# Optimization experiments

Measured on AMD Instinct MI355X. Metric: run time of the kernel, lower is better.

Reference implementation:

```python
import jax, jax.numpy as jnp
import numpy as np

D = 1280          # hidden_size
NH = 16           # num_heads
HD = 80           # head_dim
DEPTH = 4         # number of vision blocks
INTER = 3420      # mlp intermediate size
MERGE = 2         # spatial_merge_size
OUT = 3584        # merger out_hidden_size
GRID = (1, 40, 40)  # (t, h, w) patch grid -> 1600 tokens
N = GRID[0] * GRID[1] * GRID[2]
PATCH_IN = 3 * 2 * 14 * 14  # in_channels * temporal_patch * patch^2 = 1176


def _pos_emb():
    """Deterministic vision RoPE cos/sin per Qwen2_5_VLVisionModel.rot_pos_emb."""
    t, h, w = GRID
    mh, mw = h // MERGE, w // MERGE
    intra = np.arange(MERGE)
    row = np.arange(mh)[:, None, None, None] * MERGE + intra[None, None, :, None]
    col = np.arange(mw)[None, :, None, None] * MERGE + intra[None, None, None, :]
    row = np.broadcast_to(row, (mh, mw, MERGE, MERGE)).reshape(-1)
    col = np.broadcast_to(col, (mh, mw, MERGE, MERGE)).reshape(-1)
    pos = np.stack([row, col], axis=-1)        # (h*w, 2)
    if t > 1:
        pos = np.tile(pos, (t, 1))
    rot_dim = HD // 2                          # 40
    inv = 1.0 / (10000.0 ** (np.arange(0, rot_dim, 2, dtype=np.float64) / rot_dim))
    table = np.outer(np.arange(max(h, w)), inv)        # (max_hw, rot_dim//2)
    rpe = table[pos].reshape(pos.shape[0], -1)         # (N, rot_dim)
    emb = np.concatenate([rpe, rpe], axis=-1)          # (N, HD)
    return np.cos(emb).astype(np.float32), np.sin(emb).astype(np.float32)


def setup_inputs() -> dict:
    key = jax.random.key(0)
    ks = iter(jax.random.split(key, 40))
    def w(shape, s=0.02):
        return jax.random.normal(next(ks), shape, jnp.float32) * s
    cos, sin = _pos_emb()
    return dict(
        pixel_values=w((N, PATCH_IN), 1.0),
        cos=jnp.asarray(cos), sin=jnp.asarray(sin),
        patch_w=w((D, PATCH_IN)),                       # Conv3d stride==kernel -> linear
        norm1_w=jnp.ones((DEPTH, D), jnp.float32),
        qkv_w=w((DEPTH, 3 * D, D)), qkv_b=jnp.zeros((DEPTH, 3 * D), jnp.float32),
        proj_w=w((DEPTH, D, D)), proj_b=jnp.zeros((DEPTH, D), jnp.float32),
        norm2_w=jnp.ones((DEPTH, D), jnp.float32),
        gate_w=w((DEPTH, INTER, D)), gate_b=jnp.zeros((DEPTH, INTER), jnp.float32),
        up_w=w((DEPTH, INTER, D)), up_b=jnp.zeros((DEPTH, INTER), jnp.float32),
        down_w=w((DEPTH, D, INTER)), down_b=jnp.zeros((DEPTH, D), jnp.float32),
        lnq_w=jnp.ones((D,), jnp.float32),
        m1_w=w((D * MERGE ** 2, D * MERGE ** 2)), m1_b=jnp.zeros((D * MERGE ** 2,), jnp.float32),
        m2_w=w((OUT, D * MERGE ** 2)), m2_b=jnp.zeros((OUT,), jnp.float32),
    )


def _rms(x, w, eps=1e-6):
    return x * jax.lax.rsqrt(jnp.mean(x * x, axis=-1, keepdims=True) + eps) * w


def _rotate_half(x):
    x1, x2 = jnp.split(x, 2, axis=-1)
    return jnp.concatenate([-x2, x1], axis=-1)


def _forward(pixel_values, cos, sin, patch_w, norm1_w, qkv_w, qkv_b, proj_w, proj_b,
             norm2_w, gate_w, gate_b, up_w, up_b, down_w, down_b,
             lnq_w, m1_w, m1_b, m2_w, m2_b):
    # patch embed: Conv3d with kernel==stride collapses to a linear projection
    x = pixel_values @ patch_w.T                       # (N, D)
    c = cos[:, None, :]                                # (N, 1, HD)
    s = sin[:, None, :]
    scale = HD ** -0.5
    for i in range(DEPTH):
        # --- attention ---
        h = _rms(x, norm1_w[i])
        qkv = (h @ qkv_w[i].T + qkv_b[i]).reshape(N, 3, NH, HD)
        q, k, v = qkv[:, 0], qkv[:, 1], qkv[:, 2]      # (N, NH, HD)
        q = q * c + _rotate_half(q) * s
        k = k * c + _rotate_half(k) * s
        # NOTE: this impl applies NO cu_seqlens window mask -> full dense attention
        aw = jnp.einsum('nhd,mhd->hnm', q, k) * scale  # (NH, N, N)
        aw = jax.nn.softmax(aw.astype(jnp.float32), axis=-1).astype(x.dtype)
        o = jnp.einsum('hnm,mhd->nhd', aw, v).reshape(N, D)
        x = x + o @ proj_w[i].T + proj_b[i]
        # --- mlp (SwiGLU) ---
        h = _rms(x, norm2_w[i])
        g = h @ gate_w[i].T + gate_b[i]
        u = h @ up_w[i].T + up_b[i]
        x = x + (jax.nn.silu(g) * u) @ down_w[i].T + down_b[i]
    # --- patch merger ---
    h = _rms(x, lnq_w).reshape(-1, D * MERGE ** 2)      # (N/4, 5120)
    h = jax.nn.gelu(h @ m1_w.T + m1_b, approximate=False)
    return h @ m2_w.T + m2_b                            # (N/4, OUT)


def reference(pixel_values, cos, sin, patch_w, norm1_w, qkv_w, qkv_b, proj_w, proj_b,
              norm2_w, gate_w, gate_b, up_w, up_b, down_w, down_b,
              lnq_w, m1_w, m1_b, m2_w, m2_b):
    return _forward(pixel_values, cos, sin, patch_w, norm1_w, qkv_w, qkv_b, proj_w,
                    proj_b, norm2_w, gate_w, gate_b, up_w, up_b, down_w, down_b,
                    lnq_w, m1_w, m1_b, m2_w, m2_b)
```

## Files before the change

kernel.cpp:

```cpp
#include <hip/hip_runtime.h>


typedef __bf16 bf16x8 __attribute__((ext_vector_type(8)));
typedef float  f32x4  __attribute__((ext_vector_type(4)));
typedef unsigned short u16;

#define DEV __device__ __forceinline__

DEV u16 f2bf(float f) {
    union { float f; unsigned u; } v; v.f = f;
    unsigned r = v.u + 0x7FFFu + ((v.u >> 16) & 1u);
    return (u16)(r >> 16);
}
DEV float bf2f(u16 b) {
    union { float f; unsigned u; } v; v.u = ((unsigned)b) << 16; return v.f;
}

DEV void gload16(const u16* g, u16* l) {
    __builtin_amdgcn_global_load_lds(
        (const __attribute__((address_space(1))) unsigned int*)g,
        (__attribute__((address_space(3))) unsigned int*)l, 16, 0, 0);
}

enum { EPI_NONE = 0, EPI_BIAS = 1, EPI_BIAS_RESID = 2, EPI_BIAS_GELU = 3, EPI_PART = 4 };

DEV unsigned xcd_map(unsigned lin, unsigned nwg) {
    unsigned q = nwg >> 3, r = nwg & 7, xc = lin & 7, off = lin >> 3;
    return (xc < r ? xc * (q + 1) : r * (q + 1) + (xc - r) * q) + off;
}

__global__ void cvt_kernel(const float* __restrict__ src, u16* __restrict__ dst,
                           int Rs, int Cs, int Rp, int Cp,
                           long long sls, long long dls)
{
    const float* s = src + (size_t)blockIdx.y * sls;
    u16* d = dst + (size_t)blockIdx.y * dls;
    int idx = blockIdx.x * 256 + threadIdx.x;
    int cpc = Cp >> 3;
    if (idx >= Rp * cpc) return;
    int row = idx / cpc;
    int c0  = (idx - row * cpc) * 8;
    u16 v[8];
    if (row < Rs && c0 + 8 <= Cs) {
        float4 a = *reinterpret_cast<const float4*>(&s[(size_t)row * Cs + c0]);
        float4 b = *reinterpret_cast<const float4*>(&s[(size_t)row * Cs + c0 + 4]);
        v[0] = f2bf(a.x); v[1] = f2bf(a.y); v[2] = f2bf(a.z); v[3] = f2bf(a.w);
        v[4] = f2bf(b.x); v[5] = f2bf(b.y); v[6] = f2bf(b.z); v[7] = f2bf(b.w);
    } else {
#pragma unroll
        for (int j = 0; j < 8; ++j) {
            int c = c0 + j;
            v[j] = (row < Rs && c < Cs) ? f2bf(s[(size_t)row * Cs + c]) : (u16)0;
        }
    }
    *reinterpret_cast<uint4*>(&d[(size_t)row * Cp + c0]) =
        *reinterpret_cast<const uint4*>(v);
}

__global__ void gub_kernel(const float* __restrict__ gb, const float* __restrict__ ub,
                           float* __restrict__ dst)
{
    int i = blockIdx.x * 256 + threadIdx.x;
    if (i >= 4 * 6912) return;
    int l = i / 6912, c = i - l * 6912;
    float v = 0.f;
    if (c < 3456) { if (c < 3420) v = gb[l * 3420 + c]; }
    else { int c2 = c - 3456; if (c2 < 3420) v = ub[l * 3420 + c2]; }
    dst[i] = v;
}

template <int EPI, bool OF32>
__global__ __launch_bounds__(256, 3)
void gemm16_kernel(const u16* __restrict__ A, const u16* __restrict__ B,
                   const float* __restrict__ bias, const float* __restrict__ resid,
                   void* __restrict__ outp, int Kp, int ldc, int Rlim,
                   int ktn, size_t zstride)
{
    __shared__ u16 sA[3][4096];
    __shared__ u16 sB[3][4096];
    const int tid  = threadIdx.x;
    const int lane = tid & 63;
    const int w    = tid >> 6;

    const unsigned gy  = gridDim.y;
    const unsigned nwg = gridDim.x * gy;
    const unsigned lin = blockIdx.x + blockIdx.y * gridDim.x;
    const unsigned id2 = xcd_map(lin, nwg);
    const int c0 = (int)(id2 / gy) * 128;
    const int r0 = (int)(id2 - (id2 / gy) * gy) * 128;

    const int wr  = (w >> 1) * 64;
    const int wc  = (w & 1) * 64;
    const int l15 = lane & 15;
    const int kk  = (lane >> 4) * 8;
    const int pco = (((lane >> 4) ^ ((l15 >> 1) & 3)) * 8) - kk;

    const int ca  = w * 128 + lane;
    const int cb  = ca + 64;
    const int sza = ((ca & 3) ^ ((ca >> 3) & 3)) * 8;
    const int szb = ((cb & 3) ^ ((cb >> 3) & 3)) * 8;
    const size_t arow0 = (size_t)(r0 + (ca >> 2)) * Kp + sza;
    const size_t brow0 = (size_t)(c0 + (ca >> 2)) * Kp + sza;
    const size_t arow1 = (size_t)(r0 + (cb >> 2)) * Kp + szb;
    const size_t brow1 = (size_t)(c0 + (cb >> 2)) * Kp + szb;

    f32x4 acc[4][4];
#pragma unroll
    for (int i = 0; i < 4; ++i)
#pragma unroll
        for (int j = 0; j < 4; ++j) acc[i][j] = (f32x4){0.f, 0.f, 0.f, 0.f};

    const int kt0 = blockIdx.z * ktn;
    auto stage = [&](int kt, int buf) {
        int k0 = kt * 32;
        gload16(A + arow0 + k0, &sA[buf][ca * 8]);
        gload16(B + brow0 + k0, &sB[buf][ca * 8]);
        gload16(A + arow1 + k0, &sA[buf][cb * 8]);
        gload16(B + brow1 + k0, &sB[buf][cb * 8]);
    };
    auto compute = [&](int buf) {
        bf16x8 af[4], bfr[4];
#pragma unroll
        for (int f = 0; f < 4; ++f) {
            af[f]  = *reinterpret_cast<const bf16x8*>(&sA[buf][(wr + f * 16 + l15) * 32 + kk + pco]);
            bfr[f] = *reinterpret_cast<const bf16x8*>(&sB[buf][(wc + f * 16 + l15) * 32 + kk + pco]);
        }
#pragma unroll
        for (int fr = 0; fr < 4; ++fr)
#pragma unroll
            for (int fc = 0; fc < 4; ++fc)
                acc[fr][fc] = __builtin_amdgcn_mfma_f32_16x16x32_bf16(af[fr], bfr[fc], acc[fr][fc], 0, 0, 0);
    };

    const int NT = ktn;
    stage(kt0, 0);
    if (NT > 1) stage(kt0 + 1, 1);
    int bcur = 0;
    for (int t = 0; t < NT - 1; ++t) {
        asm volatile("s_waitcnt vmcnt(4)" ::: "memory");
        __builtin_amdgcn_s_barrier();
        __builtin_amdgcn_sched_barrier(0);
        if (t + 2 < NT) {
            int bn = bcur + 2; if (bn >= 3) bn -= 3;
            stage(kt0 + t + 2, bn);
        }
        __builtin_amdgcn_sched_barrier(0);
        compute(bcur);
        bcur = (bcur == 2) ? 0 : bcur + 1;
    }
    asm volatile("s_waitcnt vmcnt(0)" ::: "memory");
    __builtin_amdgcn_s_barrier();
    __builtin_amdgcn_sched_barrier(0);
    compute(bcur);

    const int rowb = r0 + wr + (lane >> 4) * 4;
    const int colb = c0 + wc + l15;
    if (EPI == EPI_PART) {
        float* pp = (float*)outp + (size_t)blockIdx.z * zstride;
#pragma unroll
        for (int fc = 0; fc < 4; ++fc) {
            int col = colb + fc * 16;
#pragma unroll
            for (int fr = 0; fr < 4; ++fr)
#pragma unroll
                for (int r2 = 0; r2 < 4; ++r2)
                    pp[(size_t)(rowb + fr * 16 + r2) * ldc + col] = acc[fr][fc][r2];
        }
        return;
    }
#pragma unroll
    for (int fc = 0; fc < 4; ++fc) {
        int col = colb + fc * 16;
        float bv = (EPI != EPI_NONE) ? bias[col] : 0.f;
#pragma unroll
        for (int fr = 0; fr < 4; ++fr) {
#pragma unroll
            for (int r2 = 0; r2 < 4; ++r2) {
                int row = rowb + fr * 16 + r2;
                if (row >= Rlim) continue;
                float v = acc[fr][fc][r2] + bv;
                if (EPI == EPI_BIAS_RESID) v += resid[(size_t)row * ldc + col];
                if (EPI == EPI_BIAS_GELU)  v = 0.5f * v * (1.f + erff(v * 0.70710678118f));
                if (OF32) ((float*)outp)[(size_t)row * ldc + col] = v;
                else      ((u16*)outp)[(size_t)row * ldc + col] = f2bf(v);
            }
        }
    }
}

template <int EPI, bool OF32>
__global__ __launch_bounds__(256, 4)
void gemm32_kernel(const u16* __restrict__ A, const u16* __restrict__ B,
                   const float* __restrict__ bias, const float* __restrict__ resid,
                   void* __restrict__ outp, int Kp, int ldc, int Rlim)
{
    __shared__ u16 sA[3][1024];
    __shared__ u16 sB[3][4096];
    const int tid  = threadIdx.x;
    const int lane = tid & 63;
    const int w    = tid >> 6;

    const unsigned gy  = gridDim.y;
    const unsigned nwg = gridDim.x * gy;
    const unsigned lin = blockIdx.x + blockIdx.y * gridDim.x;
    const unsigned id2 = xcd_map(lin, nwg);
    const int c0 = (int)(id2 / gy) * 128;
    const int r0 = (int)(id2 - (id2 / gy) * gy) * 32;

    const int wc  = w * 32;
    const int l15 = lane & 15;
    const int kk  = (lane >> 4) * 8;
    const int pco = (((lane >> 4) ^ ((l15 >> 1) & 3)) * 8) - kk;

    const int cB0 = tid, cB1 = tid + 256, cA = tid & 127;
    const size_t bsrc0 = (size_t)(c0 + (cB0 >> 2)) * Kp + ((cB0 & 3) ^ ((cB0 >> 3) & 3)) * 8;
    const size_t bsrc1 = (size_t)(c0 + (cB1 >> 2)) * Kp + ((cB1 & 3) ^ ((cB1 >> 3) & 3)) * 8;
    const size_t asrc  = (size_t)(r0 + (cA  >> 2)) * Kp + ((cA  & 3) ^ ((cA  >> 3) & 3)) * 8;

    f32x4 acc[2][2];
#pragma unroll
    for (int i = 0; i < 2; ++i)
#pragma unroll
        for (int j = 0; j < 2; ++j) acc[i][j] = (f32x4){0.f, 0.f, 0.f, 0.f};

    auto stage = [&](int kt, int buf) {
        int k0 = kt * 32;
        gload16(B + bsrc0 + k0, &sB[buf][cB0 * 8]);
        gload16(B + bsrc1 + k0, &sB[buf][cB1 * 8]);
        gload16(A + asrc  + k0, &sA[buf][cA * 8]);
    };
    auto compute = [&](int buf) {
        bf16x8 af[2], bfr[2];
#pragma unroll
        for (int f = 0; f < 2; ++f) {
            af[f]  = *reinterpret_cast<const bf16x8*>(&sA[buf][(f * 16 + l15) * 32 + kk + pco]);
            bfr[f] = *reinterpret_cast<const bf16x8*>(&sB[buf][(wc + f * 16 + l15) * 32 + kk + pco]);
        }
#pragma unroll
        for (int fr = 0; fr < 2; ++fr)
#pragma unroll
            for (int fc = 0; fc < 2; ++fc)
                acc[fr][fc] = __builtin_amdgcn_mfma_f32_16x16x32_bf16(af[fr], bfr[fc], acc[fr][fc], 0, 0, 0);
    };

    const int NT = Kp >> 5;
    stage(0, 0);
    stage(1, 1);
    int bcur = 0;
    for (int t = 0; t < NT - 1; ++t) {
        asm volatile("s_waitcnt vmcnt(3)" ::: "memory");
        __builtin_amdgcn_s_barrier();
        __builtin_amdgcn_sched_barrier(0);
        if (t + 2 < NT) {
            int bn = bcur + 2; if (bn >= 3) bn -= 3;
            stage(t + 2, bn);
        }
        __builtin_amdgcn_sched_barrier(0);
        compute(bcur);
        bcur = (bcur == 2) ? 0 : bcur + 1;
    }
    asm volatile("s_waitcnt vmcnt(0)" ::: "memory");
    __builtin_amdgcn_s_barrier();
    __builtin_amdgcn_sched_barrier(0);
    compute(bcur);

    const int rowb = r0 + (lane >> 4) * 4;
    const int colb = c0 + wc + l15;
#pragma unroll
    for (int fc = 0; fc < 2; ++fc) {
        int col = colb + fc * 16;
        float bv = (EPI != EPI_NONE) ? bias[col] : 0.f;
#pragma unroll
        for (int fr = 0; fr < 2; ++fr) {
#pragma unroll
            for (int r2 = 0; r2 < 4; ++r2) {
                int row = rowb + fr * 16 + r2;
                if (row >= Rlim) continue;
                float v = acc[fr][fc][r2] + bv;
                if (EPI == EPI_BIAS_RESID) v += resid[(size_t)row * ldc + col];
                if (EPI == EPI_BIAS_GELU)  v = 0.5f * v * (1.f + erff(v * 0.70710678118f));
                if (OF32) ((float*)outp)[(size_t)row * ldc + col] = v;
                else      ((u16*)outp)[(size_t)row * ldc + col] = f2bf(v);
            }
        }
    }
}

template <int GELU, bool OF32>
__global__ void reduce_kernel(const float* __restrict__ part, const float* __restrict__ bias,
                              void* __restrict__ outp, int C, int S, size_t zstride, int total4)
{
    int i = blockIdx.x * 256 + threadIdx.x;
    if (i >= total4) return;
    int cq = C >> 2;
    int rr = i / cq;
    int cc = (i - rr * cq) * 4;
    size_t bidx = (size_t)rr * C + cc;
    float4 s = *reinterpret_cast<const float4*>(&part[bidx]);
    for (int z = 1; z < S; ++z) {
        float4 p = *reinterpret_cast<const float4*>(&part[z * zstride + bidx]);
        s.x += p.x; s.y += p.y; s.z += p.z; s.w += p.w;
    }
    float4 b = *reinterpret_cast<const float4*>(&bias[cc]);
    s.x += b.x; s.y += b.y; s.z += b.z; s.w += b.w;
    if (GELU) {
        s.x = 0.5f * s.x * (1.f + erff(s.x * 0.70710678118f));
        s.y = 0.5f * s.y * (1.f + erff(s.y * 0.70710678118f));
        s.z = 0.5f * s.z * (1.f + erff(s.z * 0.70710678118f));
        s.w = 0.5f * s.w * (1.f + erff(s.w * 0.70710678118f));
    }
    if (OF32) {
        *reinterpret_cast<float4*>(&((float*)outp)[bidx]) = s;
    } else {
        u16 v[4] = { f2bf(s.x), f2bf(s.y), f2bf(s.z), f2bf(s.w) };
        *reinterpret_cast<uint2*>(&((u16*)outp)[bidx]) = *reinterpret_cast<const uint2*>(v);
    }
}

__global__ void rms_kernel(const float* __restrict__ x, const float* __restrict__ w,
                           u16* __restrict__ out, int cols)
{
    const int row = blockIdx.x;
    const int tid = threadIdx.x;
    const float* xr = x + (size_t)row * cols;
    float ss = 0.f;
    for (int c = tid; c < cols; c += 256) { float v = xr[c]; ss += v * v; }
#pragma unroll
    for (int m = 1; m < 64; m <<= 1) ss += __shfl_xor(ss, m);
    __shared__ float wsum[4];
    if ((tid & 63) == 0) wsum[tid >> 6] = ss;
    __syncthreads();
    float tot = wsum[0] + wsum[1] + wsum[2] + wsum[3];
    float rs = rsqrtf(tot / (float)cols + 1e-6f);
    u16* orow = out + (size_t)row * cols;
    for (int c = tid; c < cols; c += 256) orow[c] = f2bf(xr[c] * rs * w[c]);
}

__global__ void rope_kernel(u16* __restrict__ qkv, const float* __restrict__ cosb,
                            const float* __restrict__ sinb)
{
    int idx = blockIdx.x * 256 + threadIdx.x;
    int n   = idx / 640;
    int rem = idx - n * 640;
    int hh  = rem / 40;
    int d   = rem - hh * 40;
    float c0 = cosb[n * 80 + d];
    float s0 = sinb[n * 80 + d];
    float c1 = cosb[n * 80 + d + 40];
    float s1 = sinb[n * 80 + d + 40];
    size_t base = (size_t)n * 3840 + hh * 80;
    float a = bf2f(qkv[base + d]), b = bf2f(qkv[base + d + 40]);
    qkv[base + d]      = f2bf(a * c0 - b * s0);
    qkv[base + d + 40] = f2bf(b * c1 + a * s1);
    base += 1280;
    a = bf2f(qkv[base + d]); b = bf2f(qkv[base + d + 40]);
    qkv[base + d]      = f2bf(a * c0 - b * s0);
    qkv[base + d + 40] = f2bf(b * c1 + a * s1);
}

__global__ void silu_mul_kernel(const u16* __restrict__ gu, u16* __restrict__ outb)
{
    int idx = blockIdx.x * 256 + threadIdx.x;
    if (idx >= 1664 * 432) return;
    int row = idx / 432, c8 = (idx - row * 432) * 8;
    u16 gv[8], uv[8];
    *reinterpret_cast<uint4*>(gv) = *reinterpret_cast<const uint4*>(&gu[(size_t)row * 6912 + c8]);
    *reinterpret_cast<uint4*>(uv) = *reinterpret_cast<const uint4*>(&gu[(size_t)row * 6912 + 3456 + c8]);
#pragma unroll
    for (int j = 0; j < 8; ++j) {
        float x = bf2f(gv[j]);
        gv[j] = f2bf(x / (1.f + __expf(-x)) * bf2f(uv[j]));
    }
    *reinterpret_cast<uint4*>(&outb[(size_t)row * 3456 + c8]) = *reinterpret_cast<const uint4*>(gv);
}

__global__ __launch_bounds__(256, 2)
void attn_kernel(const u16* __restrict__ qkv, u16* __restrict__ o)
{
    __shared__ __align__(16) u16      Klds[2][64][104];
    __shared__ __align__(16) unsigned Vt32[2][80][36];
    __shared__ __align__(16) u16      Plds[4][16][72];
    const int tid  = threadIdx.x;
    const int lane = tid & 63;
    const int w    = tid >> 6;
    const int l15  = lane & 15;
    const int kk   = (lane >> 4) * 8;
    unsigned lin = blockIdx.y * 25 + blockIdx.x;
    unsigned id2 = (lin & 7) * 50 + (lin >> 3);
    const int hh = (int)(id2 / 25);
    const int qt = (int)(id2 - hh * 25);
    const float scale = 0.11180339887498949f;

    const int koff = 1280 + hh * 80;
    const int voff = 2560 + hh * 80;

    {
        int r  = tid >> 2;
        int cq = 80 + (tid & 3) * 4;
        *reinterpret_cast<uint2*>(&Klds[0][r][cq]) = make_uint2(0u, 0u);
        *reinterpret_cast<uint2*>(&Klds[1][r][cq]) = make_uint2(0u, 0u);
    }

    const int qrow = qt * 64 + w * 16 + l15;
    bf16x8 aq[3];
#pragma unroll
    for (int s = 0; s < 3; ++s) {
        int d = 32 * s + kk;
        union { bf16x8 v; uint4 q; } uu;
        if (d < 80) uu.q = *reinterpret_cast<const uint4*>(&qkv[(size_t)qrow * 3840 + hh * 80 + d]);
        else        uu.q = make_uint4(0u, 0u, 0u, 0u);
        aq[s] = uu.v;
    }

    const int kc0 = tid, kc1 = tid + 256, kc2 = tid + 512;
    const int kr0 = kc0 / 10, k80 = (kc0 - kr0 * 10) * 8;
    const int kr1 = kc1 / 10, k81 = (kc1 - kr1 * 10) * 8;
    const int kr2 = kc2 / 10, k82 = (kc2 - kr2 * 10) * 8;
    const size_t ksrc0 = (size_t)kr0 * 3840 + koff + k80;
    const size_t ksrc1 = (size_t)kr1 * 3840 + koff + k81;
    const size_t ksrc2 = (size_t)kr2 * 3840 + koff + k82;
    const int rpA = tid & 31, gA = tid >> 5;
    const int gB = 8 + (tid >> 5);
    const size_t vsrcA = (size_t)(2 * rpA) * 3840 + voff + gA * 8;
    const size_t vsrcB = (size_t)(2 * rpA) * 3840 + voff + gB * 8;

    uint4 kg0, kg1, kg2, va0, va1, vb0, vb1;
    auto LOADR = [&](int kb) {
        size_t tb = (size_t)kb * 245760;
        kg0 = *reinterpret_cast<const uint4*>(&qkv[tb + ksrc0]);
        kg1 = *reinterpret_cast<const uint4*>(&qkv[tb + ksrc1]);
        if (tid < 128) kg2 = *reinterpret_cast<const uint4*>(&qkv[tb + ksrc2]);
        va0 = *reinterpret_cast<const uint4*>(&qkv[tb + vsrcA]);
        va1 = *reinterpret_cast<const uint4*>(&qkv[tb + vsrcA + 3840]);
        if (tid < 64) {
            vb0 = *reinterpret_cast<const uint4*>(&qkv[tb + vsrcB]);
            vb1 = *reinterpret_cast<const uint4*>(&qkv[tb + vsrcB + 3840]);
        }
    };
    auto STORE = [&](int b) {
        *reinterpret_cast<uint4*>(&Klds[b][kr0][k80]) = kg0;
        *reinterpret_cast<uint4*>(&Klds[b][kr1][k81]) = kg1;
        if (tid < 128) *reinterpret_cast<uint4*>(&Klds[b][kr2][k82]) = kg2;
        union { uint4 q; u16 h[8]; } xa0, xa1;
        xa0.q = va0; xa1.q = va1;
#pragma unroll
        for (int j = 0; j < 8; ++j)
            Vt32[b][gA * 8 + j][rpA] = (unsigned)xa0.h[j] | ((unsigned)xa1.h[j] << 16);
        if (tid < 64) {
            union { uint4 q; u16 h[8]; } xb0, xb1;
            xb0.q = vb0; xb1.q = vb1;
#pragma unroll
            for (int j = 0; j < 8; ++j)
                Vt32[b][gB * 8 + j][rpA] = (unsigned)xb0.h[j] | ((unsigned)xb1.h[j] << 16);
        }
    };

    f32x4 acc_o[5];
#pragma unroll
    for (int fd = 0; fd < 5; ++fd) acc_o[fd] = (f32x4){0.f, 0.f, 0.f, 0.f};
    float m[4], lsum[4];
#pragma unroll
    for (int r2 = 0; r2 < 4; ++r2) { m[r2] = -__builtin_inff(); lsum[r2] = 0.f; }

    LOADR(0);
    STORE(0);
    __syncthreads();
    int cur = 0;

    for (int kb = 0; kb < 25; ++kb) {
        if (kb < 24) LOADR(kb + 1);

        f32x4 sf[4];
#pragma unroll
        for (int fc = 0; fc < 4; ++fc) {
            f32x4 c = (f32x4){0.f, 0.f, 0.f, 0.f};
#pragma unroll
            for (int s = 0; s < 3; ++s)
                c = __builtin_amdgcn_mfma_f32_16x16x32_bf16(
                        aq[s],
                        *reinterpret_cast<const bf16x8*>(&Klds[cur][fc * 16 + l15][32 * s + kk]),
                        c, 0, 0, 0);
            sf[fc] = c * scale;
        }

        float mx[4];
#pragma unroll
        for (int r2 = 0; r2 < 4; ++r2)
            mx[r2] = fmaxf(fmaxf(sf[0][r2], sf[1][r2]), fmaxf(sf[2][r2], sf[3][r2]));
#pragma unroll
        for (int msk = 1; msk <= 8; msk <<= 1)
#pragma unroll
            for (int r2 = 0; r2 < 4; ++r2)
                mx[r2] = fmaxf(mx[r2], __shfl_xor(mx[r2], msk));
        float alpha[4];
#pragma unroll
        for (int r2 = 0; r2 < 4; ++r2) {
            float mn = fmaxf(m[r2], mx[r2]);
            alpha[r2] = __expf(m[r2] - mn);
            m[r2] = mn;
        }
        float psum[4] = {0.f, 0.f, 0.f, 0.f};
#pragma unroll
        for (int fc = 0; fc < 4; ++fc)
#pragma unroll
            for (int r2 = 0; r2 < 4; ++r2) {
                float p = __expf(sf[fc][r2] - m[r2]);
                sf[fc][r2] = p;
                psum[r2] += p;
            }
#pragma unroll
        for (int msk = 1; msk <= 8; msk <<= 1)
#pragma unroll
            for (int r2 = 0; r2 < 4; ++r2) psum[r2] += __shfl_xor(psum[r2], msk);
#pragma unroll
        for (int r2 = 0; r2 < 4; ++r2) lsum[r2] = lsum[r2] * alpha[r2] + psum[r2];
#pragma unroll
        for (int fd = 0; fd < 5; ++fd)
#pragma unroll
            for (int r2 = 0; r2 < 4; ++r2) acc_o[fd][r2] *= alpha[r2];

        const int prow = (lane >> 4) * 4;
#pragma unroll
        for (int fc = 0; fc < 4; ++fc)
#pragma unroll
            for (int r2 = 0; r2 < 4; ++r2)
                Plds[w][prow + r2][fc * 16 + l15] = f2bf(sf[fc][r2]);

        bf16x8 ap[2];
#pragma unroll
        for (int ks = 0; ks < 2; ++ks)
            ap[ks] = *reinterpret_cast<const bf16x8*>(&Plds[w][l15][32 * ks + kk]);
#pragma unroll
        for (int fd = 0; fd < 5; ++fd) {
            const u16* vrow = reinterpret_cast<const u16*>(&Vt32[cur][fd * 16 + l15][0]);
#pragma unroll
            for (int ks = 0; ks < 2; ++ks)
                acc_o[fd] = __builtin_amdgcn_mfma_f32_16x16x32_bf16(
                        ap[ks],
                        *reinterpret_cast<const bf16x8*>(&vrow[32 * ks + kk]),
                        acc_o[fd], 0, 0, 0);
        }

        if (kb < 24) STORE(cur ^ 1);
        __syncthreads();
        cur ^= 1;
    }

    float inv[4];
#pragma unroll
    for (int r2 = 0; r2 < 4; ++r2) inv[r2] = 1.f / lsum[r2];
    const int orow = qt * 64 + w * 16 + (lane >> 4) * 4;
    const int ocol = hh * 80 + l15;
#pragma unroll
    for (int fd = 0; fd < 5; ++fd)
#pragma unroll
        for (int r2 = 0; r2 < 4; ++r2)
            o[(size_t)(orow + r2) * 1280 + ocol + fd * 16] = f2bf(acc_o[fd][r2] * inv[r2]);
}

extern "C" void kernel_launch(void* const* d_in, const int* in_sizes, int n_in,
                              void* d_out, int out_size, void* d_ws, size_t ws_size,
                              hipStream_t stream)
{
    const float* pixel  = (const float*)d_in[0];
    const float* cosb   = (const float*)d_in[1];
    const float* sinb   = (const float*)d_in[2];
    const float* patchw = (const float*)d_in[3];
    const float* n1w    = (const float*)d_in[4];
    const float* qkvw   = (const float*)d_in[5];
    const float* qkvb   = (const float*)d_in[6];
    const float* projw  = (const float*)d_in[7];
    const float* projb  = (const float*)d_in[8];
    const float* n2w    = (const float*)d_in[9];
    const float* gatew  = (const float*)d_in[10];
    const float* gateb  = (const float*)d_in[11];
    const float* upw    = (const float*)d_in[12];
    const float* upb    = (const float*)d_in[13];
    const float* downw  = (const float*)d_in[14];
    const float* downb  = (const float*)d_in[15];
    const float* lnqw   = (const float*)d_in[16];
    const float* m1w    = (const float*)d_in[17];
    const float* m1b    = (const float*)d_in[18];
    const float* m2w    = (const float*)d_in[19];
    const float* m2b    = (const float*)d_in[20];
    float* out = (float*)d_out;

    char* base = (char*)d_ws;
    float* x      = (float*)(base);
    u16*   h      = (u16*)(base + 8519680);
    u16*   qbuf   = (u16*)(base + 12779520);
    u16*   pix16  = qbuf;
    u16*   gsep   = (u16*)(base + 25559040);
    u16*   o      = gsep;
    u16*   pw16   = gsep;
    u16*   gu     = (u16*)(base + 37060608);
    u16*   t1     = gu;
    float* guB    = (float*)(base + 60063744);
    u16*   qkvw16 = (u16*)(base + 60174336);
    u16*   projw16= (u16*)(base + 99495936);
    u16*   guw16  = (u16*)(base + 112603136);
    u16*   downw16= (u16*)(base + 183382016);
    u16*   m1w16  = guw16;
    u16*   m2w16  = (u16*)(base + 112603136 + 52428800);
    float* part   = (float*)qkvw16;

    dim3 blk(256);
    auto cvb = [](int Rp, int Cp) { return (Rp * (Cp >> 3) + 255) / 256; };

    cvt_kernel<<<dim3(cvb(1664,1216),1), blk, 0, stream>>>(pixel, pix16, 1600, 1176, 1664, 1216, 0, 0);
    cvt_kernel<<<dim3(cvb(1280,1216),1), blk, 0, stream>>>(patchw, pw16, 1280, 1176, 1280, 1216, 0, 0);
    cvt_kernel<<<dim3(cvb(15360,1280),1), blk, 0, stream>>>(qkvw, qkvw16, 15360, 1280, 15360, 1280, 0, 0);
    cvt_kernel<<<dim3(cvb(5120,1280),1), blk, 0, stream>>>(projw, projw16, 5120, 1280, 5120, 1280, 0, 0);
    cvt_kernel<<<dim3(cvb(3456,1280),4), blk, 0, stream>>>(gatew, guw16, 3420, 1280, 3456, 1280, 4377600LL, 8847360LL);
    cvt_kernel<<<dim3(cvb(3456,1280),4), blk, 0, stream>>>(upw, guw16 + 4423680, 3420, 1280, 3456, 1280, 4377600LL, 8847360LL);
    cvt_kernel<<<dim3(cvb(1280,3456),4), blk, 0, stream>>>(downw, downw16, 1280, 3420, 1280, 3456, 4377600LL, 4423680LL);
    gub_kernel<<<108, blk, 0, stream>>>(gateb, upb, guB);

    gemm32_kernel<EPI_NONE, true><<<dim3(10,52), blk, 0, stream>>>(pix16, pw16, nullptr, nullptr, x, 1216, 1280, 1664);
    for (int i = 0; i < 4; ++i) {
        rms_kernel<<<1600, blk, 0, stream>>>(x, n1w + i*1280, h, 1280);
        gemm16_kernel<EPI_BIAS, false><<<dim3(30,13), blk, 0, stream>>>(h, qkvw16 + (size_t)i*4915200, qkvb + i*3840, nullptr, qbuf, 1280, 3840, 1664, 40, 0);
        rope_kernel<<<4000, blk, 0, stream>>>(qbuf, cosb, sinb);
        attn_kernel<<<dim3(25,16), blk, 0, stream>>>(qbuf, o);
        gemm32_kernel<EPI_BIAS_RESID, true><<<dim3(10,52), blk, 0, stream>>>(o, projw16 + (size_t)i*1638400, projb + i*1280, x, x, 1280, 1280, 1664);
        rms_kernel<<<1600, blk, 0, stream>>>(x, n2w + i*1280, h, 1280);
        gemm16_kernel<EPI_BIAS, false><<<dim3(54,13), blk, 0, stream>>>(h, guw16 + (size_t)i*8847360, guB + i*6912, nullptr, gu, 1280, 6912, 1664, 40, 0);
        silu_mul_kernel<<<2808, blk, 0, stream>>>(gu, gsep);
        gemm32_kernel<EPI_BIAS_RESID, true><<<dim3(10,52), blk, 0, stream>>>(gsep, downw16 + (size_t)i*4423680, downb + i*1280, x, x, 3456, 1280, 1664);
    }
    cvt_kernel<<<dim3(cvb(5120,5120),1), blk, 0, stream>>>(m1w, m1w16, 5120, 5120, 5120, 5120, 0, 0);
    cvt_kernel<<<dim3(cvb(3584,5120),1), blk, 0, stream>>>(m2w, m2w16, 3584, 5120, 3584, 5120, 0, 0);
    rms_kernel<<<1600, blk, 0, stream>>>(x, lnqw, h, 1280);
    gemm16_kernel<EPI_PART, false><<<dim3(40,4,5), blk, 0, stream>>>(h, m1w16, nullptr, nullptr, part, 5120, 5120, 512, 32, 2621440);
    reduce_kernel<1, false><<<2560, blk, 0, stream>>>(part, m1b, t1, 5120, 5, 2621440, 655360);
    gemm16_kernel<EPI_PART, false><<<dim3(28,4,5), blk, 0, stream>>>(t1, m2w16, nullptr, nullptr, part, 5120, 3584, 512, 32, 1835008);
    reduce_kernel<0, true><<<1400, blk, 0, stream>>>(part, m2b, out, 3584, 5, 1835008, 358400);
}
```

Measured before the change: 1.293 ms.

## Fuse fp32-to-bf16 weight conversion into GEMM B-tile loads

Removes the separate weight conversion kernels. The GEMMs now read fp32 weights directly, convert them to bf16 in registers and write them to shared memory. The A operand still uses async global-to-LDS loads, but the pipeline drops from triple to double buffering with plain __syncthreads. This saves a full pass that reads fp32 weights and writes bf16 copies. In exchange, each GEMM must read weights at twice the bytes, and every block that shares a weight tile repeats the conversion. Padded rows and columns are handled by predicated loads and zero fill.

```diff
diff --git a/kernel.cpp b/kernel.cpp
--- a/kernel.cpp
+++ b/kernel.cpp
@@ -30,11 +30,8 @@
 }
 
 __global__ void cvt_kernel(const float* __restrict__ src, u16* __restrict__ dst,
-                           int Rs, int Cs, int Rp, int Cp,
-                           long long sls, long long dls)
-{
-    const float* s = src + (size_t)blockIdx.y * sls;
-    u16* d = dst + (size_t)blockIdx.y * dls;
+                           int Rs, int Cs, int Rp, int Cp)
+{
     int idx = blockIdx.x * 256 + threadIdx.x;
     int cpc = Cp >> 3;
     if (idx >= Rp * cpc) return;
@@ -42,18 +39,18 @@
     int c0  = (idx - row * cpc) * 8;
     u16 v[8];
     if (row < Rs && c0 + 8 <= Cs) {
-        float4 a = *reinterpret_cast<const float4*>(&s[(size_t)row * Cs + c0]);
-        float4 b = *reinterpret_cast<const float4*>(&s[(size_t)row * Cs + c0 + 4]);
+        float4 a = *reinterpret_cast<const float4*>(&src[(size_t)row * Cs + c0]);
+        float4 b = *reinterpret_cast<const float4*>(&src[(size_t)row * Cs + c0 + 4]);
         v[0] = f2bf(a.x); v[1] = f2bf(a.y); v[2] = f2bf(a.z); v[3] = f2bf(a.w);
         v[4] = f2bf(b.x); v[5] = f2bf(b.y); v[6] = f2bf(b.z); v[7] = f2bf(b.w);
     } else {
 #pragma unroll
         for (int j = 0; j < 8; ++j) {
             int c = c0 + j;
-            v[j] = (row < Rs && c < Cs) ? f2bf(s[(size_t)row * Cs + c]) : (u16)0;
-        }
-    }
-    *reinterpret_cast<uint4*>(&d[(size_t)row * Cp + c0]) =
+            v[j] = (row < Rs && c < Cs) ? f2bf(src[(size_t)row * Cs + c]) : (u16)0;
+        }
+    }
+    *reinterpret_cast<uint4*>(&dst[(size_t)row * Cp + c0]) =
         *reinterpret_cast<const uint4*>(v);
 }
 
@@ -71,13 +68,15 @@
 
 template <int EPI, bool OF32>
 __global__ __launch_bounds__(256, 3)
-void gemm16_kernel(const u16* __restrict__ A, const u16* __restrict__ B,
-                   const float* __restrict__ bias, const float* __restrict__ resid,
-                   void* __restrict__ outp, int Kp, int ldc, int Rlim,
-                   int ktn, size_t zstride)
-{
-    __shared__ u16 sA[3][4096];
-    __shared__ u16 sB[3][4096];
+void gemm16f_kernel(const u16* __restrict__ A, const float* __restrict__ B0,
+                    const float* __restrict__ B1, int Bsplit, int BvalidRows,
+                    int KpA, int Klog,
+                    const float* __restrict__ bias, const float* __restrict__ resid,
+                    void* __restrict__ outp, int ldc, int Rlim,
+                    int ktn, size_t zstride)
+{
+    __shared__ u16 sA[2][4096];
+    __shared__ u16 sB[2][4096];
     const int tid  = threadIdx.x;
     const int lane = tid & 63;
     const int w    = tid >> 6;
@@ -95,14 +94,25 @@
     const int kk  = (lane >> 4) * 8;
     const int pco = (((lane >> 4) ^ ((l15 >> 1) & 3)) * 8) - kk;
 
-    const int ca  = w * 128 + lane;
-    const int cb  = ca + 64;
-    const int sza = ((ca & 3) ^ ((ca >> 3) & 3)) * 8;
-    const int szb = ((cb & 3) ^ ((cb >> 3) & 3)) * 8;
-    const size_t arow0 = (size_t)(r0 + (ca >> 2)) * Kp + sza;
-    const size_t brow0 = (size_t)(c0 + (ca >> 2)) * Kp + sza;
-    const size_t arow1 = (size_t)(r0 + (cb >> 2)) * Kp + szb;
-    const size_t brow1 = (size_t)(c0 + (cb >> 2)) * Kp + szb;
+    const int ca0 = tid, ca1 = tid + 256;
+    const int ar0 = ca0 >> 2, ar1 = ca1 >> 2;
+    const int alq0 = ((ca0 & 3) ^ ((ar0 >> 1) & 3)) * 8;
+    const int alq1 = ((ca1 & 3) ^ ((ar1 >> 1) & 3)) * 8;
+    const size_t asrc0 = (size_t)(r0 + ar0) * KpA + alq0;
+    const size_t asrc1 = (size_t)(r0 + ar1) * KpA + alq1;
+
+    const int cb0 = tid, cb1 = tid + 256;
+    const int br0 = cb0 >> 2, br1 = cb1 >> 2;
+    const int blq0 = ((cb0 & 3) ^ ((br0 >> 1) & 3)) * 8;
+    const int blq1 = ((cb1 & 3) ^ ((br1 >> 1) & 3)) * 8;
+    bool bv0, bv1;
+    const float *bp0, *bp1;
+    {
+        int gr = c0 + br0; int hs = gr >= Bsplit; int lr = gr - (hs ? Bsplit : 0);
+        bv0 = lr < BvalidRows; bp0 = (hs ? B1 : B0) + (size_t)lr * Klog + blq0;
+        gr = c0 + br1; hs = gr >= Bsplit; lr = gr - (hs ? Bsplit : 0);
+        bv1 = lr < BvalidRows; bp1 = (hs ? B1 : B0) + (size_t)lr * Klog + blq1;
+    }
 
     f32x4 acc[4][4];
 #pragma unroll
@@ -111,19 +121,36 @@
         for (int j = 0; j < 4; ++j) acc[i][j] = (f32x4){0.f, 0.f, 0.f, 0.f};
 
     const int kt0 = blockIdx.z * ktn;
-    auto stage = [&](int kt, int buf) {
+    float4 f00, f01, f10, f11;
+    auto LOADB = [&](int kt) {
         int k0 = kt * 32;
-        gload16(A + arow0 + k0, &sA[buf][ca * 8]);
-        gload16(B + brow0 + k0, &sB[buf][ca * 8]);
-        gload16(A + arow1 + k0, &sA[buf][cb * 8]);
-        gload16(B + brow1 + k0, &sB[buf][cb * 8]);
-    };
-    auto compute = [&](int buf) {
+        if (bv0) { f00 = *reinterpret_cast<const float4*>(bp0 + k0);
+                   f01 = *reinterpret_cast<const float4*>(bp0 + k0 + 4); }
+        else     { f00 = make_float4(0.f,0.f,0.f,0.f); f01 = f00; }
+        if (bv1) { f10 = *reinterpret_cast<const float4*>(bp1 + k0);
+                   f11 = *reinterpret_cast<const float4*>(bp1 + k0 + 4); }
+        else     { f10 = make_float4(0.f,0.f,0.f,0.f); f11 = f10; }
+    };
+    auto WRITEB = [&](int s) {
+        u16 h8[8];
+        h8[0]=f2bf(f00.x); h8[1]=f2bf(f00.y); h8[2]=f2bf(f00.z); h8[3]=f2bf(f00.w);
+        h8[4]=f2bf(f01.x); h8[5]=f2bf(f01.y); h8[6]=f2bf(f01.z); h8[7]=f2bf(f01.w);
+        *reinterpret_cast<uint4*>(&sB[s][cb0 * 8]) = *reinterpret_cast<const uint4*>(h8);
+        h8[0]=f2bf(f10.x); h8[1]=f2bf(f10.y); h8[2]=f2bf(f10.z); h8[3]=f2bf(f10.w);
+        h8[4]=f2bf(f11.x); h8[5]=f2bf(f11.y); h8[6]=f2bf(f11.z); h8[7]=f2bf(f11.w);
+        *reinterpret_cast<uint4*>(&sB[s][cb1 * 8]) = *reinterpret_cast<const uint4*>(h8);
+    };
+    auto stageA = [&](int kt, int s) {
+        int k0 = kt * 32;
+        gload16(A + asrc0 + k0, &sA[s][ca0 * 8]);
+        gload16(A + asrc1 + k0, &sA[s][ca1 * 8]);
+    };
+    auto compute = [&](int s) {
         bf16x8 af[4], bfr[4];
 #pragma unroll
         for (int f = 0; f < 4; ++f) {
-            af[f]  = *reinterpret_cast<const bf16x8*>(&sA[buf][(wr + f * 16 + l15) * 32 + kk + pco]);
-            bfr[f] = *reinterpret_cast<const bf16x8*>(&sB[buf][(wc + f * 16 + l15) * 32 + kk + pco]);
+            af[f]  = *reinterpret_cast<const bf16x8*>(&sA[s][(wr + f * 16 + l15) * 32 + kk + pco]);
+            bfr[f] = *reinterpret_cast<const bf16x8*>(&sB[s][(wc + f * 16 + l15) * 32 + kk + pco]);
         }
 #pragma unroll
         for (int fr = 0; fr < 4; ++fr)
@@ -133,25 +160,20 @@
     };
 
     const int NT = ktn;
-    stage(kt0, 0);
-    if (NT > 1) stage(kt0 + 1, 1);
-    int bcur = 0;
-    for (int t = 0; t < NT - 1; ++t) {
-        asm volatile("s_waitcnt vmcnt(4)" ::: "memory");
-        __builtin_amdgcn_s_barrier();
-        __builtin_amdgcn_sched_barrier(0);
-        if (t + 2 < NT) {
-            int bn = bcur + 2; if (bn >= 3) bn -= 3;
-            stage(kt0 + t + 2, bn);
-        }
-        __builtin_amdgcn_sched_barrier(0);
-        compute(bcur);
-        bcur = (bcur == 2) ? 0 : bcur + 1;
-    }
-    asm volatile("s_waitcnt vmcnt(0)" ::: "memory");
-    __builtin_amdgcn_s_barrier();
-    __builtin_amdgcn_sched_barrier(0);
-    compute(bcur);
+    LOADB(kt0);
+    stageA(kt0, 0);
+    WRITEB(0);
+    stageA(kt0 + 1, 1);
+    LOADB(kt0 + 1);
+    __syncthreads();
+    int s = 0;
+    for (int t = 0; t < NT; ++t) {
+        compute(s);
+        if (t + 1 < NT) WRITEB(s ^ 1);
+        __syncthreads();
+        if (t + 2 < NT) { stageA(kt0 + t + 2, s); LOADB(kt0 + t + 2); }
+        s ^= 1;
+    }
 
     const int rowb = r0 + wr + (lane >> 4) * 4;
     const int colb = c0 + wc + l15;
@@ -190,12 +212,13 @@
 
 template <int EPI, bool OF32>
 __global__ __launch_bounds__(256, 4)
-void gemm32_kernel(const u16* __restrict__ A, const u16* __restrict__ B,
-                   const float* __restrict__ bias, const float* __restrict__ resid,
-                   void* __restrict__ outp, int Kp, int ldc, int Rlim)
-{
-    __shared__ u16 sA[3][1024];
-    __shared__ u16 sB[3][4096];
+void gemm32f_kernel(const u16* __restrict__ A, const float* __restrict__ B,
+                    int KpA, int Klog,
+                    const float* __restrict__ bias, const float* __restrict__ resid,
+                    void* __restrict__ outp, int ldc, int Rlim)
+{
+    __shared__ u16 sA[2][1024];
+    __shared__ u16 sB[2][4096];
     const int tid  = threadIdx.x;
     const int lane = tid & 63;
     const int w    = tid >> 6;
@@ -212,10 +235,17 @@
     const int kk  = (lane >> 4) * 8;
     const int pco = (((lane >> 4) ^ ((l15 >> 1) & 3)) * 8) - kk;
 
-    const int cB0 = tid, cB1 = tid + 256, cA = tid & 127;
-    const size_t bsrc0 = (size_t)(c0 + (cB0 >> 2)) * Kp + ((cB0 & 3) ^ ((cB0 >> 3) & 3)) * 8;
-    const size_t bsrc1 = (size_t)(c0 + (cB1 >> 2)) * Kp + ((cB1 & 3) ^ ((cB1 >> 3) & 3)) * 8;
-    const size_t asrc  = (size_t)(r0 + (cA  >> 2)) * Kp + ((cA  & 3) ^ ((cA  >> 3) & 3)) * 8;
+    const int ca = tid & 127;
+    const int aro = ca >> 2;
+    const int alq = ((ca & 3) ^ ((aro >> 1) & 3)) * 8;
+    const size_t asrc = (size_t)(r0 + aro) * KpA + alq;
+
+    const int cb0 = tid, cb1 = tid + 256;
+    const int br0 = cb0 >> 2, br1 = cb1 >> 2;
+    const int blq0 = ((cb0 & 3) ^ ((br0 >> 1) & 3)) * 8;
+    const int blq1 = ((cb1 & 3) ^ ((br1 >> 1) & 3)) * 8;
+    const float* bp0 = B + (size_t)(c0 + br0) * Klog;
+    const float* bp1 = B + (size_t)(c0 + br1) * Klog;
 
     f32x4 acc[2][2];
 #pragma unroll
@@ -223,18 +253,42 @@
 #pragma unroll
         for (int j = 0; j < 2; ++j) acc[i][j] = (f32x4){0.f, 0.f, 0.f, 0.f};
 
-    auto stage = [&](int kt, int buf) {
+    float4 f00, f01, f10, f11;
+    auto ldchunk = [&](const float* bp, int ks, float4& a, float4& b) {
+        if (ks + 8 <= Klog) {
+            a = *reinterpret_cast<const float4*>(bp + ks);
+            b = *reinterpret_cast<const float4*>(bp + ks + 4);
+        } else {
+            float t[8];
+#pragma unroll
+            for (int e = 0; e < 8; ++e) t[e] = (ks + e < Klog) ? bp[ks + e] : 0.f;
+            a = make_float4(t[0], t[1], t[2], t[3]);
+            b = make_float4(t[4], t[5], t[6], t[7]);
+        }
+    };
+    auto LOADB = [&](int kt) {
         int k0 = kt * 32;
-        gload16(B + bsrc0 + k0, &sB[buf][cB0 * 8]);
-        gload16(B + bsrc1 + k0, &sB[buf][cB1 * 8]);
-        gload16(A + asrc  + k0, &sA[buf][cA * 8]);
-    };
-    auto compute = [&](int buf) {
+        ldchunk(bp0, k0 + blq0, f00, f01);
+        ldchunk(bp1, k0 + blq1, f10, f11);
+    };
+    auto WRITEB = [&](int s) {
+        u16 h8[8];
+        h8[0]=f2bf(f00.x); h8[1]=f2bf(f00.y); h8[2]=f2bf(f00.z); h8[3]=f2bf(f00.w);
+        h8[4]=f2bf(f01.x); h8[5]=f2bf(f01.y); h8[6]=f2bf(f01.z); h8[7]=f2bf(f01.w);
+        *reinterpret_cast<uint4*>(&sB[s][cb0 * 8]) = *reinterpret_cast<const uint4*>(h8);
+        h8[0]=f2bf(f10.x); h8[1]=f2bf(f10.y); h8[2]=f2bf(f10.z); h8[3]=f2bf(f10.w);
+        h8[4]=f2bf(f11.x); h8[5]=f2bf(f11.y); h8[6]=f2bf(f11.z); h8[7]=f2bf(f11.w);
+        *reinterpret_cast<uint4*>(&sB[s][cb1 * 8]) = *reinterpret_cast<const uint4*>(h8);
+    };
+    auto stageA = [&](int kt, int s) {
+        if (tid < 128) gload16(A + asrc + kt * 32, &sA[s][ca * 8]);
+    };
+    auto compute = [&](int s) {
         bf16x8 af[2], bfr[2];
 #pragma unroll
         for (int f = 0; f < 2; ++f) {
-            af[f]  = *reinterpret_cast<const bf16x8*>(&sA[buf][(f * 16 + l15) * 32 + kk + pco]);
-            bfr[f] = *reinterpret_cast<const bf16x8*>(&sB[buf][(wc + f * 16 + l15) * 32 + kk + pco]);
+            af[f]  = *reinterpret_cast<const bf16x8*>(&sA[s][(f * 16 + l15) * 32 + kk + pco]);
+            bfr[f] = *reinterpret_cast<const bf16x8*>(&sB[s][(wc + f * 16 + l15) * 32 + kk + pco]);
         }
 #pragma unroll
         for (int fr = 0; fr < 2; ++fr)
@@ -243,26 +297,21 @@
                 acc[fr][fc] = __builtin_amdgcn_mfma_f32_16x16x32_bf16(af[fr], bfr[fc], acc[fr][fc], 0, 0, 0);
     };
 
-    const int NT = Kp >> 5;
-    stage(0, 0);
-    stage(1, 1);
-    int bcur = 0;
-    for (int t = 0; t < NT - 1; ++t) {
-        asm volatile("s_waitcnt vmcnt(3)" ::: "memory");
-        __builtin_amdgcn_s_barrier();
-        __builtin_amdgcn_sched_barrier(0);
-        if (t + 2 < NT) {
-            int bn = bcur + 2; if (bn >= 3) bn -= 3;
-            stage(t + 2, bn);
-        }
-        __builtin_amdgcn_sched_barrier(0);
-        compute(bcur);
-        bcur = (bcur == 2) ? 0 : bcur + 1;
-    }
-    asm volatile("s_waitcnt vmcnt(0)" ::: "memory");
-    __builtin_amdgcn_s_barrier();
-    __builtin_amdgcn_sched_barrier(0);
-    compute(bcur);
+    const int NT = KpA >> 5;
+    LOADB(0);
+    stageA(0, 0);
+    WRITEB(0);
+    stageA(1, 1);
+    LOADB(1);
+    __syncthreads();
+    int s = 0;
+    for (int t = 0; t < NT; ++t) {
+        compute(s);
+        if (t + 1 < NT) WRITEB(s ^ 1);
+        __syncthreads();
+        if (t + 2 < NT) { stageA(t + 2, s); LOADB(t + 2); }
+        s ^= 1;
+    }
 
     const int rowb = r0 + (lane >> 4) * 4;
     const int colb = c0 + wc + l15;
@@ -586,53 +635,51 @@
     float* out = (float*)d_out;
 
     char* base = (char*)d_ws;
-    float* x      = (float*)(base);
-    u16*   h      = (u16*)(base + 8519680);
-    u16*   qbuf   = (u16*)(base + 12779520);
-    u16*   pix16  = qbuf;
-    u16*   gsep   = (u16*)(base + 25559040);
-    u16*   o      = gsep;
-    u16*   pw16   = gsep;
-    u16*   gu     = (u16*)(base + 37060608);
-    u16*   t1     = gu;
-    float* guB    = (float*)(base + 60063744);
-    u16*   qkvw16 = (u16*)(base + 60174336);
-    u16*   projw16= (u16*)(base + 99495936);
-    u16*   guw16  = (u16*)(base + 112603136);
-    u16*   downw16= (u16*)(base + 183382016);
-    u16*   m1w16  = guw16;
-    u16*   m2w16  = (u16*)(base + 112603136 + 52428800);
-    float* part   = (float*)qkvw16;
+    float* x    = (float*)(base);
+    u16*   h    = (u16*)(base + 8519680);
+    u16*   qbuf = (u16*)(base + 12779520);
+    u16*   pix16= (u16*)(base + 25559040);
+    u16*   gsep = (u16*)(base + 29499392);
+    u16*   o    = gsep;
+    u16*   gu   = (u16*)(base + 41000960);
+    u16*   t1   = gu;
+    float* guB  = (float*)(base + 64004096);
+    float* part = (float*)(base + 64114688);
 
     dim3 blk(256);
-    auto cvb = [](int Rp, int Cp) { return (Rp * (Cp >> 3) + 255) / 256; };
-
-    cvt_kernel<<<dim3(cvb(1664,1216),1), blk, 0, stream>>>(pixel, pix16, 1600, 1176, 1664, 1216, 0, 0);
-    cvt_kernel<<<dim3(cvb(1280,1216),1), blk, 0, stream>>>(patchw, pw16, 1280, 1176, 1280, 1216, 0, 0);
-    cvt_kernel<<<dim3(cvb(15360,1280),1), blk, 0, stream>>>(qkvw, qkvw16, 15360, 1280, 15360, 1280, 0, 0);
-    cvt_kernel<<<dim3(cvb(5120,1280),1), blk, 0, stream>>>(projw, projw16, 5120, 1280, 5120, 1280, 0, 0);
-    cvt_kernel<<<dim3(cvb(3456,1280),4), blk, 0, stream>>>(gatew, guw16, 3420, 1280, 3456, 1280, 4377600LL, 8847360LL);
-    cvt_kernel<<<dim3(cvb(3456,1280),4), blk, 0, stream>>>(upw, guw16 + 4423680, 3420, 1280, 3456, 1280, 4377600LL, 8847360LL);
-    cvt_kernel<<<dim3(cvb(1280,3456),4), blk, 0, stream>>>(downw, downw16, 1280, 3420, 1280, 3456, 4377600LL, 4423680LL);
+    const int BIG = 1 << 28;
+
+    cvt_kernel<<<963, blk, 0, stream>>>(pixel, pix16, 1600, 1176, 1664, 1184);
     gub_kernel<<<108, blk, 0, stream>>>(gateb, upb, guB);
 
-    gemm32_kernel<EPI_NONE, true><<<dim3(10,52), blk, 0, stream>>>(pix16, pw16, nullptr, nullptr, x, 1216, 1280, 1664);
+    gemm32f_kernel<EPI_NONE, true><<<dim3(10,52), blk, 0, stream>>>(
+        pix16, patchw, 1184, 1176, nullptr, nullptr, x, 1280, 1664);
     for (int i = 0; i < 4; ++i) {
         rms_kernel<<<1600, blk, 0, stream>>>(x, n1w + i*1280, h, 1280);
-        gemm16_kernel<EPI_BIAS, false><<<dim3(30,13), blk, 0, stream>>>(h, qkvw16 + (size_t)i*4915200, qkvb + i*3840, nullptr, qbuf, 1280, 3840, 1664, 40, 0);
+        gemm16f_kernel<EPI_BIAS, false><<<dim3(30,13), blk, 0, stream>>>(
+            h, qkvw + (size_t)i*4915200, nullptr, BIG, BIG, 1280, 1280,
+            qkvb + i*3840, nullptr, qbuf, 3840, 1664, 40, 0);
         rope_kernel<<<4000, blk, 0, stream>>>(qbuf, cosb, sinb);
         attn_kernel<<<dim3(25,16), blk, 0, stream>>>(qbuf, o);
-        gemm32_kernel<EPI_BIAS_RESID, true><<<dim3(10,52), blk, 0, stream>>>(o, projw16 + (size_t)i*1638400, projb + i*1280, x, x, 1280, 1280, 1664);
+        gemm32f_kernel<EPI_BIAS_RESID, true><<<dim3(10,52), blk, 0, stream>>>(
+            o, projw + (size_t)i*1638400, 1280, 1280,
+            projb + i*1280, x, x, 1280, 1664);
         rms_kernel<<<1600, blk, 0, stream>>>(x, n2w + i*1280, h, 1280);
-        gemm16_kernel<EPI_BIAS, false><<<dim3(54,13), blk, 0, stream>>>(h, guw16 + (size_t)i*8847360, guB + i*6912, nullptr, gu, 1280, 6912, 1664, 40, 0);
+        gemm16f_kernel<EPI_BIAS, false><<<dim3(54,13), blk, 0, stream>>>(
+            h, gatew + (size_t)i*4377600, upw + (size_t)i*4377600, 3456, 3420, 1280, 1280,
+            guB + i*6912, nullptr, gu, 6912, 1664, 40, 0);
         silu_mul_kernel<<<2808, blk, 0, stream>>>(gu, gsep);
-        gemm32_kernel<EPI_BIAS_RESID, true><<<dim3(10,52), blk, 0, stream>>>(gsep, downw16 + (size_t)i*4423680, downb + i*1280, x, x, 3456, 1280, 1664);
-    }
-    cvt_kernel<<<dim3(cvb(5120,5120),1), blk, 0, stream>>>(m1w, m1w16, 5120, 5120, 5120, 5120, 0, 0);
-    cvt_kernel<<<dim3(cvb(3584,5120),1), blk, 0, stream>>>(m2w, m2w16, 3584, 5120, 3584, 5120, 0, 0);
+        gemm32f_kernel<EPI_BIAS_RESID, true><<<dim3(10,52), blk, 0, stream>>>(
+            gsep, downw + (size_t)i*4377600, 3456, 3420,
+            downb + i*1280, x, x, 1280, 1664);
+    }
     rms_kernel<<<1600, blk, 0, stream>>>(x, lnqw, h, 1280);
-    gemm16_kernel<EPI_PART, false><<<dim3(40,4,5), blk, 0, stream>>>(h, m1w16, nullptr, nullptr, part, 5120, 5120, 512, 32, 2621440);
+    gemm16f_kernel<EPI_PART, false><<<dim3(40,4,5), blk, 0, stream>>>(
+        h, m1w, nullptr, BIG, BIG, 5120, 5120,
+        nullptr, nullptr, part, 5120, 512, 32, 2621440);
     reduce_kernel<1, false><<<2560, blk, 0, stream>>>(part, m1b, t1, 5120, 5, 2621440, 655360);
-    gemm16_kernel<EPI_PART, false><<<dim3(28,4,5), blk, 0, stream>>>(t1, m2w16, nullptr, nullptr, part, 5120, 3584, 512, 32, 1835008);
+    gemm16f_kernel<EPI_PART, false><<<dim3(28,4,5), blk, 0, stream>>>(
+        t1, m2w, nullptr, BIG, BIG, 5120, 5120,
+        nullptr, nullptr, part, 3584, 512, 32, 1835008);
     reduce_kernel<0, true><<<1400, blk, 0, stream>>>(part, m2b, out, 3584, 5, 1835008, 358400);
 }
```

Result: slower. 2.262 ms (+74.9%).
